# Kernel optimization log

Hardware: AMD Instinct MI355X
Metric: run time of the kernel (lower is better)

The kernel has to match this reference:

```python
import jax, jax.numpy as jnp
import numpy as np
import math

B, N, D, SEQ = 4, 1024, 512, 256
HID, DIST_D, N_NER, N_LAB = 150, 128, 3, 4
SPANS_PER_WORD = 0.5
ASPECT, OPINION = 1, 2
NUM_DIST_EMB = 512


def setup_inputs() -> dict:
    key = jax.random.key(0)
    ks = jax.random.split(key, 9)
    starts = jax.random.randint(ks[0], (B, N), 0, SEQ)
    widths = jax.random.randint(ks[1], (B, N), 0, 8)
    ends = jnp.clip(starts + widths, 0, SEQ - 1)
    spans = jnp.stack([starts, ends], axis=-1).astype(jnp.int32)  # [B,N,2]
    ner_scores = jax.random.normal(ks[2], (B, N, N_NER), jnp.float32)
    span_embeddings = jax.random.normal(ks[3], (B, N, D), jnp.float32)
    span_mask = jnp.ones((B, N), dtype=bool)

    pair_dim = 2 * D + DIST_D

    def xavier(k, shape):
        std = math.sqrt(2.0 / (shape[0] + shape[1]))
        return jax.random.normal(k, shape, jnp.float32) * std

    dist_table = xavier(ks[4], (NUM_DIST_EMB, DIST_D))
    W1 = xavier(ks[5], (pair_dim, HID)); b1 = jnp.zeros((HID,), jnp.float32)
    W2 = xavier(ks[6], (HID, HID));      b2 = jnp.zeros((HID,), jnp.float32)
    Wc = xavier(ks[7], (HID, N_LAB));    bc = jnp.zeros((N_LAB,), jnp.float32)

    return dict(spans=spans, ner_scores=ner_scores, span_embeddings=span_embeddings,
                span_mask=span_mask, seq_length=SEQ, dist_table=dist_table,
                W1=W1, b1=b1, W2=W2, b2=b2, Wc=Wc, bc=bc)


def bucket_values(d, num_identity=4, num_total=10):
    # semi-logscale buckets: [0,1,2,3,4,5-7,8-15,16-31,32-63,64+]
    logspace = jnp.floor(jnp.log2(jnp.maximum(d, 1).astype(jnp.float32))).astype(jnp.int32) + (num_identity - 1)
    return jnp.clip(jnp.where(d <= num_identity, d, logspace), 0, num_total - 1)


def _prune(scores, mask, k):
    masked = jnp.where(mask, scores, jnp.float32(-1e20))
    _, idx = jax.lax.top_k(masked, k)  # [B,k]
    return idx


def reference(spans, ner_scores, span_embeddings, span_mask, seq_length,
              dist_table, W1, b1, W2, b2, Wc, bc):
    bsz, n_spans, d = span_embeddings.shape
    k = min(int(math.ceil(seq_length * SPANS_PER_WORD)), n_spans)

    a_idx = _prune(ner_scores[..., ASPECT], span_mask, k)    # [B,k]
    o_idx = _prune(ner_scores[..., OPINION], span_mask, k)
    a_keep = jnp.ones((bsz, k), dtype=bool)  # uniform seq_length -> all kept
    o_keep = a_keep

    gather = lambda t, i: jnp.take_along_axis(t, i[..., None], axis=1)
    a_emb = gather(span_embeddings, a_idx)   # [B,k,D]
    o_emb = gather(span_embeddings, o_idx)   # [B,k,D]
    spans_a = gather(spans, a_idx)           # [B,k,2]
    spans_o = gather(spans, o_idx)           # [B,k,2]

    # pairwise min span distance -> bucket -> embedding
    dis1 = jnp.abs(spans_a[..., 0][:, :, None] - spans_o[..., 1][:, None, :])
    dis2 = jnp.abs(spans_a[..., 1][:, :, None] - spans_o[..., 0][:, None, :])
    dis = jnp.minimum(dis1, dis2)                      # [B,k,k]
    dist_emb = dist_table[bucket_values(dis)]          # [B,k,k,DIST_D]

    pair = jnp.concatenate([
        jnp.broadcast_to(a_emb[:, :, None, :], (bsz, k, k, d)),
        jnp.broadcast_to(o_emb[:, None, :, :], (bsz, k, k, d)),
        dist_emb,
    ], axis=-1)                                        # [B,k,k,2D+DIST_D]

    # FeedForward (2 layers, ReLU, dropout=identity at eval) + classifier
    h = jax.nn.relu(pair @ W1 + b1)
    h = jax.nn.relu(h @ W2 + b2)
    scores = h @ Wc + bc                               # [B,k,k,n_labels]

    rel_mask = a_keep[:, :, None] & o_keep[:, None, :]
    return (jax.nn.softmax(scores, axis=-1), rel_mask, pair, spans_a, spans_o)
```

## Files before the change

kernel.cpp:

```cpp
#include <hip/hip_runtime.h>
#include <hip/hip_bf16.h>

#define BB 4
#define NN 1024
#define DD 512
#define KK 128
#define HID 150
#define HIDP 160
#define W2TS 176
#define DIST_D 128
#define PAIRD 1152

typedef __attribute__((ext_vector_type(4))) float f32x4;
typedef __attribute__((ext_vector_type(8))) short s16x8;

__device__ __forceinline__ int bucket_of(int dd) {
    return (dd <= 4) ? dd : min(34 - __clz(dd), 9);
}

__global__ __launch_bounds__(256) void k_topk(const int* __restrict__ spans,
                                              const float* __restrict__ ner,
                                              const float* __restrict__ dist_table,
                                              const float* __restrict__ W1,
                                              const float* __restrict__ b1,
                                              const float* __restrict__ W2,
                                              int* ws_aidx, int* ws_oidx,
                                              int* ws_sa, int* ws_so,
                                              float* ws_cd, __hip_bfloat16* ws_w2t,
                                              float* out3, float* out4) {
    int t = threadIdx.x;
    int bx = blockIdx.x;
    if (bx < 32) {
        __shared__ unsigned long long sk[NN];
        int b = bx >> 3;
        int which = (bx >> 2) & 1;
        int chunk = bx & 3;
        int ch = which ? 2 : 1;
#pragma unroll
        for (int k = 0; k < 4; ++k) {
            int d = k * 256 + t;
            float v = ner[(b * NN + d) * 3 + ch];
            unsigned int u = __float_as_uint(v);
            unsigned int s = (u & 0x80000000u) ? ~u : (u ^ 0x80000000u);
            sk[d] = ((unsigned long long)s << 32) | (unsigned int)(NN - 1 - d);
        }
        __syncthreads();
        int idx = chunk * 256 + t;
        unsigned long long mine = sk[idx];
        int cnt = 0;
#pragma unroll 16
        for (int d = 0; d < NN; ++d) cnt += (sk[d] > mine) ? 1 : 0;
        if (cnt < KK) {
            int s0 = spans[(b * NN + idx) * 2];
            int s1 = spans[(b * NN + idx) * 2 + 1];
            int row = b * KK + cnt;
            if (which == 0) {
                ws_aidx[row] = idx;
                ws_sa[row * 2] = s0; ws_sa[row * 2 + 1] = s1;
                out3[row * 2] = (float)s0; out3[row * 2 + 1] = (float)s1;
            } else {
                ws_oidx[row] = idx;
                ws_so[row * 2] = s0; ws_so[row * 2 + 1] = s1;
                out4[row * 2] = (float)s0; out4[row * 2 + 1] = (float)s1;
            }
        }
    } else if (bx < 42) {
        int bk = bx - 32;
        if (t < HIDP) {
            float acc = 0.f;
            if (t < HID) {
                acc = b1[t];
                for (int d = 0; d < DIST_D; ++d)
                    acc = fmaf(dist_table[bk * DIST_D + d], W1[(size_t)(2 * DD + d) * HID + t], acc);
            }
            ws_cd[bk * HIDP + t] = acc;
        }
    } else {
        int e = (bx - 42) * 256 + t;
        if (e < HIDP * W2TS) {
            int n = e / W2TS, d = e - n * W2TS;
            float v = (n < HID && d < HID) ? W2[d * HID + n] : 0.f;
            ws_w2t[e] = __float2bfloat16(v);
        }
    }
}

__global__ __launch_bounds__(256) void k_contrib(const float* __restrict__ emb,
                                                 const float* __restrict__ W1,
                                                 const int* __restrict__ ws_aidx,
                                                 const int* __restrict__ ws_oidx,
                                                 float* ws_ca, float* ws_co) {
    __shared__ __align__(16) float es[4][DD];
    int t = threadIdx.x;
    int bx = blockIdx.x;
    int which = bx >> 7;
    int row0 = (bx & 127) * 4;
    const int* idxsrc = which ? ws_oidx : ws_aidx;
    for (int x = t; x < 512; x += 256) {
        int r = x >> 7, c = x & 127;
        int row = row0 + r;
        int b = row >> 7;
        int idx = idxsrc[row];
        ((float4*)es[r])[c] = ((const float4*)(emb + ((size_t)(b * NN) + idx) * DD))[c];
    }
    __syncthreads();
    if (t < HIDP) {
        float a0 = 0.f, a1 = 0.f, a2 = 0.f, a3 = 0.f;
        if (t < HID) {
            const float* w = W1 + (size_t)(which * DD) * HID + t;
#pragma unroll 4
            for (int d4 = 0; d4 < 128; ++d4) {
                float4 e0 = ((const float4*)es[0])[d4];
                float4 e1 = ((const float4*)es[1])[d4];
                float4 e2 = ((const float4*)es[2])[d4];
                float4 e3 = ((const float4*)es[3])[d4];
                float w0 = w[(size_t)(4 * d4 + 0) * HID];
                float w1v = w[(size_t)(4 * d4 + 1) * HID];
                float w2v = w[(size_t)(4 * d4 + 2) * HID];
                float w3 = w[(size_t)(4 * d4 + 3) * HID];
                a0 = fmaf(e0.x, w0, a0); a0 = fmaf(e0.y, w1v, a0); a0 = fmaf(e0.z, w2v, a0); a0 = fmaf(e0.w, w3, a0);
                a1 = fmaf(e1.x, w0, a1); a1 = fmaf(e1.y, w1v, a1); a1 = fmaf(e1.z, w2v, a1); a1 = fmaf(e1.w, w3, a1);
                a2 = fmaf(e2.x, w0, a2); a2 = fmaf(e2.y, w1v, a2); a2 = fmaf(e2.z, w2v, a2); a2 = fmaf(e2.w, w3, a2);
                a3 = fmaf(e3.x, w0, a3); a3 = fmaf(e3.y, w1v, a3); a3 = fmaf(e3.z, w2v, a3); a3 = fmaf(e3.w, w3, a3);
            }
        }
        float* dstb = which ? ws_co : ws_ca;
        dstb[(row0 + 0) * HIDP + t] = a0;
        dstb[(row0 + 1) * HIDP + t] = a1;
        dstb[(row0 + 2) * HIDP + t] = a2;
        dstb[(row0 + 3) * HIDP + t] = a3;
    }
}

__global__ __launch_bounds__(256, 2) void k_fused(const float* __restrict__ emb,
                                                  const float* __restrict__ dist_table,
                                                  const float* __restrict__ Wc,
                                                  const float* __restrict__ bcp,
                                                  const float* __restrict__ b2p,
                                                  const int* __restrict__ ws_aidx,
                                                  const int* __restrict__ ws_oidx,
                                                  const int* __restrict__ ws_sa,
                                                  const int* __restrict__ ws_so,
                                                  const float* __restrict__ ws_ca,
                                                  const float* __restrict__ ws_co,
                                                  const float* __restrict__ ws_cd,
                                                  const __hip_bfloat16* __restrict__ ws_w2t,
                                                  float* __restrict__ out0,
                                                  float* __restrict__ out1,
                                                  float* __restrict__ out2) {
    int t = threadIdx.x;
    int bx = blockIdx.x;

    if (bx >= 1024) {
        int i = (bx - 1024) * 256 + t;
        ((float4*)out1)[i] = make_float4(1.f, 1.f, 1.f, 1.f);
        return;
    }

    if ((bx & 1) == 0) {
        int bi = bx >> 1;
        int b = bi >> 7;
        int wave = t >> 6, l = t & 63;
        int lc = l & 15, lg = l >> 4;
        int r0 = wave * 32 + lc, r1 = r0 + 16;

        int sa0 = ws_sa[bi * 2], sa1 = ws_sa[bi * 2 + 1];
        int so00 = ws_so[(b * KK + r0) * 2], so01 = ws_so[(b * KK + r0) * 2 + 1];
        int so10 = ws_so[(b * KK + r1) * 2], so11 = ws_so[(b * KK + r1) * 2 + 1];
        int bkt0 = bucket_of(min(abs(sa0 - so01), abs(sa1 - so00)));
        int bkt1 = bucket_of(min(abs(sa0 - so11), abs(sa1 - so10)));

        const f32x4* ca4 = (const f32x4*)(ws_ca + (size_t)bi * HIDP);
        const f32x4* co04 = (const f32x4*)(ws_co + (size_t)(b * KK + r0) * HIDP);
        const f32x4* co14 = (const f32x4*)(ws_co + (size_t)(b * KK + r1) * HIDP);
        const f32x4* cd04 = (const f32x4*)(ws_cd + (size_t)bkt0 * HIDP);
        const f32x4* cd14 = (const f32x4*)(ws_cd + (size_t)bkt1 * HIDP);

        s16x8 af0[5], af1[5];
        union U8 { s16x8 frag; __hip_bfloat16 h[8]; };
#pragma unroll
        for (int kk = 0; kk < 5; ++kk) {
            int o = kk * 8 + lg * 2;
            f32x4 caa = ca4[o], cab = ca4[o + 1];
            f32x4 s0a = caa + co04[o] + cd04[o];
            f32x4 s0b = cab + co04[o + 1] + cd04[o + 1];
            f32x4 s1a = caa + co14[o] + cd14[o];
            f32x4 s1b = cab + co14[o + 1] + cd14[o + 1];
            U8 u0, u1;
#pragma unroll
            for (int e = 0; e < 4; ++e) {
                u0.h[e]     = __float2bfloat16(fmaxf(s0a[e], 0.f));
                u0.h[e + 4] = __float2bfloat16(fmaxf(s0b[e], 0.f));
                u1.h[e]     = __float2bfloat16(fmaxf(s1a[e], 0.f));
                u1.h[e + 4] = __float2bfloat16(fmaxf(s1b[e], 0.f));
            }
            af0[kk] = u0.frag;
            af1[kk] = u1.frag;
        }

        f32x4 acc[2][10];
#pragma unroll
        for (int mi = 0; mi < 2; ++mi)
#pragma unroll
            for (int nt = 0; nt < 10; ++nt)
                acc[mi][nt] = (f32x4){0.f, 0.f, 0.f, 0.f};

#pragma unroll
        for (int kk = 0; kk < 5; ++kk) {
#pragma unroll
            for (int nt = 0; nt < 10; ++nt) {
                s16x8 bf = *(const s16x8*)&ws_w2t[(nt * 16 + lc) * W2TS + kk * 32 + lg * 8];
                acc[0][nt] = __builtin_amdgcn_mfma_f32_16x16x32_bf16(af0[kk], bf, acc[0][nt], 0, 0, 0);
                acc[1][nt] = __builtin_amdgcn_mfma_f32_16x16x32_bf16(af1[kk], bf, acc[1][nt], 0, 0, 0);
            }
        }

        float4 wcv[10];
        float b2v[10];
#pragma unroll
        for (int nt = 0; nt < 10; ++nt) {
            int n = nt * 16 + lc;
            if (n < HID) {
                wcv[nt] = *(const float4*)(Wc + n * 4);
                b2v[nt] = b2p[n];
            } else {
                wcv[nt] = make_float4(0.f, 0.f, 0.f, 0.f);
                b2v[nt] = 0.f;
            }
        }
        float bc0 = bcp[0], bc1 = bcp[1], bc2 = bcp[2], bc3 = bcp[3];

#pragma unroll
        for (int mi = 0; mi < 2; ++mi) {
#pragma unroll
            for (int r = 0; r < 4; ++r) {
                int j = wave * 32 + mi * 16 + lg * 4 + r;
                float p0 = 0.f, p1 = 0.f, p2 = 0.f, p3 = 0.f;
#pragma unroll
                for (int nt = 0; nt < 10; ++nt) {
                    float h2 = fmaxf(acc[mi][nt][r] + b2v[nt], 0.f);
                    p0 = fmaf(h2, wcv[nt].x, p0);
                    p1 = fmaf(h2, wcv[nt].y, p1);
                    p2 = fmaf(h2, wcv[nt].z, p2);
                    p3 = fmaf(h2, wcv[nt].w, p3);
                }
#pragma unroll
                for (int m = 8; m >= 1; m >>= 1) {
                    p0 += __shfl_xor(p0, m, 16);
                    p1 += __shfl_xor(p1, m, 16);
                    p2 += __shfl_xor(p2, m, 16);
                    p3 += __shfl_xor(p3, m, 16);
                }
                p0 += bc0; p1 += bc1; p2 += bc2; p3 += bc3;
                float mx = fmaxf(fmaxf(p0, p1), fmaxf(p2, p3));
                float e0 = expf(p0 - mx), e1 = expf(p1 - mx), e2 = expf(p2 - mx), e3 = expf(p3 - mx);
                float inv = 1.f / (e0 + e1 + e2 + e3);
                if (lc < 4) {
                    float v = (lc == 0) ? e0 : (lc == 1) ? e1 : (lc == 2) ? e2 : e3;
                    out0[((size_t)bi * KK + j) * 4 + lc] = v * inv;
                }
            }
        }
    } else {
        int pid = bx >> 1;
        int b = pid >> 7;
        int ig = (pid >> 2) & 31;
        int jc = pid & 3;
        int i0 = ig << 2;
        int j0 = jc << 5;
        int c = t & 127;
        int half = t >> 7;

        const f32x4* ebase = (const f32x4*)(emb + (size_t)b * NN * DD);

        f32x4 areg[4];
#pragma unroll
        for (int ii = 0; ii < 4; ++ii) {
            int aidx = ws_aidx[b * KK + i0 + ii];
            areg[ii] = ebase[(size_t)aidx * 128 + c];
        }

        f32x4 oreg[16];
#pragma unroll
        for (int it = 0; it < 16; ++it) {
            int j = it * 2 + half;
            int oidx = ws_oidx[b * KK + j0 + j];
            oreg[it] = ebase[(size_t)oidx * 128 + c];
        }

        int dj[4], dc[4], so0v[4], so1v[4];
#pragma unroll
        for (int it = 0; it < 4; ++it) {
            int x = it * 256 + t;
            dj[it] = x >> 5; dc[it] = x & 31;
            so0v[it] = ws_so[(b * KK + j0 + dj[it]) * 2];
            so1v[it] = ws_so[(b * KK + j0 + dj[it]) * 2 + 1];
        }
        f32x4 dreg[4][4];
#pragma unroll
        for (int ii = 0; ii < 4; ++ii) {
            int sa0 = ws_sa[(b * KK + i0 + ii) * 2];
            int sa1 = ws_sa[(b * KK + i0 + ii) * 2 + 1];
#pragma unroll
            for (int it = 0; it < 4; ++it) {
                int bkt = bucket_of(min(abs(sa0 - so1v[it]), abs(sa1 - so0v[it])));
                dreg[ii][it] = ((const f32x4*)dist_table)[bkt * 32 + dc[it]];
            }
        }

#pragma unroll
        for (int ii = 0; ii < 4; ++ii) {
            f32x4* dst = (f32x4*)(out2 + (size_t)(b * KK + i0 + ii) * (KK * PAIRD))
                         + (size_t)j0 * 288;
#pragma unroll
            for (int it = 0; it < 16; ++it) {
                int j = it * 2 + half;
                dst[j * 288 + c] = areg[ii];
                dst[j * 288 + 128 + c] = oreg[it];
            }
#pragma unroll
            for (int it = 0; it < 4; ++it)
                dst[dj[it] * 288 + 256 + dc[it]] = dreg[ii][it];
        }
    }
}

extern "C" void kernel_launch(void* const* d_in, const int* in_sizes, int n_in,
                              void* d_out, int out_size, void* d_ws, size_t ws_size,
                              hipStream_t stream) {
    const int*   spans = (const int*)d_in[0];
    const float* ner   = (const float*)d_in[1];
    const float* emb   = (const float*)d_in[2];
    const float* dist_table = (const float*)d_in[5];
    const float* W1 = (const float*)d_in[6];
    const float* b1 = (const float*)d_in[7];
    const float* W2 = (const float*)d_in[8];
    const float* b2 = (const float*)d_in[9];
    const float* Wc = (const float*)d_in[10];
    const float* bc = (const float*)d_in[11];

    float* out0 = (float*)d_out;
    float* out1 = out0 + (size_t)BB * KK * KK * 4;
    float* out2 = out1 + (size_t)BB * KK * KK;
    float* out3 = out2 + (size_t)BB * KK * KK * PAIRD;
    float* out4 = out3 + (size_t)BB * KK * 2;

    int* ws_aidx = (int*)d_ws;
    int* ws_oidx = ws_aidx + BB * KK;
    int* ws_sa   = ws_oidx + BB * KK;
    int* ws_so   = ws_sa + BB * KK * 2;
    float* ws_ca = (float*)(ws_so + BB * KK * 2);
    float* ws_co = ws_ca + BB * KK * HIDP;
    float* ws_cd = ws_co + BB * KK * HIDP;
    __hip_bfloat16* ws_w2t = (__hip_bfloat16*)(ws_cd + 16 * HIDP);

    k_topk<<<152, 256, 0, stream>>>(spans, ner, dist_table, W1, b1, W2,
                                    ws_aidx, ws_oidx, ws_sa, ws_so,
                                    ws_cd, ws_w2t, out3, out4);
    k_contrib<<<256, 256, 0, stream>>>(emb, W1, ws_aidx, ws_oidx, ws_ca, ws_co);
    k_fused<<<1088, 256, 0, stream>>>(emb, dist_table, Wc, bc, b2,
                                      ws_aidx, ws_oidx, ws_sa, ws_so,
                                      ws_ca, ws_co, ws_cd, ws_w2t,
                                      out0, out1, out2);
}
```

Baseline: 97.95 us.

## Rebalance pair-tensor writes across middle and main kernels to overlap with contrib

The pair-tensor materialisation is moved into a shared device function. A quarter of its blocks (128), plus the ones-mask fill, now run in the middle kernel alongside the W1 contribution GEMV, which by itself only used 256 blocks. The remaining 384 pair blocks run first in the main kernel, ahead of the MFMA classifier blocks, which are no longer interleaved with them. The aim is to fill idle CUs during the small contrib kernel and shorten the main kernel, at the cost of a heavier middle kernel whose pair blocks use more registers (launch_bounds 256,2).

```diff
diff --git a/kernel.cpp b/kernel.cpp
--- a/kernel.cpp
+++ b/kernel.cpp
@@ -16,6 +16,75 @@
 
 __device__ __forceinline__ int bucket_of(int dd) {
     return (dd <= 4) ? dd : min(34 - __clz(dd), 9);
+}
+
+__device__ __forceinline__ void pair_body(int pid, int t,
+                                          const float* __restrict__ emb,
+                                          const float* __restrict__ dist_table,
+                                          const int* __restrict__ ws_aidx,
+                                          const int* __restrict__ ws_oidx,
+                                          const int* __restrict__ ws_sa,
+                                          const int* __restrict__ ws_so,
+                                          float* __restrict__ out2) {
+    int b = pid >> 7;
+    int ig = (pid >> 2) & 31;
+    int jc = pid & 3;
+    int i0 = ig << 2;
+    int j0 = jc << 5;
+    int c = t & 127;
+    int half = t >> 7;
+
+    const f32x4* ebase = (const f32x4*)(emb + (size_t)b * NN * DD);
+
+    f32x4 areg[4];
+#pragma unroll
+    for (int ii = 0; ii < 4; ++ii) {
+        int aidx = ws_aidx[b * KK + i0 + ii];
+        areg[ii] = ebase[(size_t)aidx * 128 + c];
+    }
+
+    f32x4 oreg[16];
+#pragma unroll
+    for (int it = 0; it < 16; ++it) {
+        int j = it * 2 + half;
+        int oidx = ws_oidx[b * KK + j0 + j];
+        oreg[it] = ebase[(size_t)oidx * 128 + c];
+    }
+
+    int dj[4], dc[4], so0v[4], so1v[4];
+#pragma unroll
+    for (int it = 0; it < 4; ++it) {
+        int x = it * 256 + t;
+        dj[it] = x >> 5; dc[it] = x & 31;
+        so0v[it] = ws_so[(b * KK + j0 + dj[it]) * 2];
+        so1v[it] = ws_so[(b * KK + j0 + dj[it]) * 2 + 1];
+    }
+    f32x4 dreg[4][4];
+#pragma unroll
+    for (int ii = 0; ii < 4; ++ii) {
+        int sa0 = ws_sa[(b * KK + i0 + ii) * 2];
+        int sa1 = ws_sa[(b * KK + i0 + ii) * 2 + 1];
+#pragma unroll
+        for (int it = 0; it < 4; ++it) {
+            int bkt = bucket_of(min(abs(sa0 - so1v[it]), abs(sa1 - so0v[it])));
+            dreg[ii][it] = ((const f32x4*)dist_table)[bkt * 32 + dc[it]];
+        }
+    }
+
+#pragma unroll
+    for (int ii = 0; ii < 4; ++ii) {
+        f32x4* dst = (f32x4*)(out2 + (size_t)(b * KK + i0 + ii) * (KK * PAIRD))
+                     + (size_t)j0 * 288;
+#pragma unroll
+        for (int it = 0; it < 16; ++it) {
+            int j = it * 2 + half;
+            dst[j * 288 + c] = areg[ii];
+            dst[j * 288 + 128 + c] = oreg[it];
+        }
+#pragma unroll
+        for (int it = 0; it < 4; ++it)
+            dst[dj[it] * 288 + 256 + dc[it]] = dreg[ii][it];
+    }
 }
 
 __global__ __launch_bounds__(256) void k_topk(const int* __restrict__ spans,
@@ -85,16 +154,33 @@
     }
 }
 
-__global__ __launch_bounds__(256) void k_contrib(const float* __restrict__ emb,
-                                                 const float* __restrict__ W1,
-                                                 const int* __restrict__ ws_aidx,
-                                                 const int* __restrict__ ws_oidx,
-                                                 float* ws_ca, float* ws_co) {
+__global__ __launch_bounds__(256, 2) void k_mid(const float* __restrict__ emb,
+                                                const float* __restrict__ dist_table,
+                                                const float* __restrict__ W1,
+                                                const int* __restrict__ ws_aidx,
+                                                const int* __restrict__ ws_oidx,
+                                                const int* __restrict__ ws_sa,
+                                                const int* __restrict__ ws_so,
+                                                float* ws_ca, float* ws_co,
+                                                float* __restrict__ out1,
+                                                float* __restrict__ out2) {
     __shared__ __align__(16) float es[4][DD];
     int t = threadIdx.x;
     int bx = blockIdx.x;
-    int which = bx >> 7;
-    int row0 = (bx & 127) * 4;
+
+    if (bx < 128) {
+        pair_body(bx, t, emb, dist_table, ws_aidx, ws_oidx, ws_sa, ws_so, out2);
+        return;
+    }
+    if (bx >= 384) {
+        int i = (bx - 384) * 256 + t;
+        ((float4*)out1)[i] = make_float4(1.f, 1.f, 1.f, 1.f);
+        return;
+    }
+
+    int cbx = bx - 128;
+    int which = cbx >> 7;
+    int row0 = (cbx & 127) * 4;
     const int* idxsrc = which ? ws_oidx : ws_aidx;
     for (int x = t; x < 512; x += 256) {
         int r = x >> 7, c = x & 127;
@@ -132,195 +218,130 @@
     }
 }
 
-__global__ __launch_bounds__(256, 2) void k_fused(const float* __restrict__ emb,
-                                                  const float* __restrict__ dist_table,
-                                                  const float* __restrict__ Wc,
-                                                  const float* __restrict__ bcp,
-                                                  const float* __restrict__ b2p,
-                                                  const int* __restrict__ ws_aidx,
-                                                  const int* __restrict__ ws_oidx,
-                                                  const int* __restrict__ ws_sa,
-                                                  const int* __restrict__ ws_so,
-                                                  const float* __restrict__ ws_ca,
-                                                  const float* __restrict__ ws_co,
-                                                  const float* __restrict__ ws_cd,
-                                                  const __hip_bfloat16* __restrict__ ws_w2t,
-                                                  float* __restrict__ out0,
-                                                  float* __restrict__ out1,
-                                                  float* __restrict__ out2) {
+__global__ __launch_bounds__(256, 2) void k_main(const float* __restrict__ emb,
+                                                 const float* __restrict__ dist_table,
+                                                 const float* __restrict__ Wc,
+                                                 const float* __restrict__ bcp,
+                                                 const float* __restrict__ b2p,
+                                                 const int* __restrict__ ws_aidx,
+                                                 const int* __restrict__ ws_oidx,
+                                                 const int* __restrict__ ws_sa,
+                                                 const int* __restrict__ ws_so,
+                                                 const float* __restrict__ ws_ca,
+                                                 const float* __restrict__ ws_co,
+                                                 const float* __restrict__ ws_cd,
+                                                 const __hip_bfloat16* __restrict__ ws_w2t,
+                                                 float* __restrict__ out0,
+                                                 float* __restrict__ out2) {
     int t = threadIdx.x;
     int bx = blockIdx.x;
 
-    if (bx >= 1024) {
-        int i = (bx - 1024) * 256 + t;
-        ((float4*)out1)[i] = make_float4(1.f, 1.f, 1.f, 1.f);
+    if (bx < 384) {
+        pair_body(128 + bx, t, emb, dist_table, ws_aidx, ws_oidx, ws_sa, ws_so, out2);
         return;
     }
 
-    if ((bx & 1) == 0) {
-        int bi = bx >> 1;
-        int b = bi >> 7;
-        int wave = t >> 6, l = t & 63;
-        int lc = l & 15, lg = l >> 4;
-        int r0 = wave * 32 + lc, r1 = r0 + 16;
-
-        int sa0 = ws_sa[bi * 2], sa1 = ws_sa[bi * 2 + 1];
-        int so00 = ws_so[(b * KK + r0) * 2], so01 = ws_so[(b * KK + r0) * 2 + 1];
-        int so10 = ws_so[(b * KK + r1) * 2], so11 = ws_so[(b * KK + r1) * 2 + 1];
-        int bkt0 = bucket_of(min(abs(sa0 - so01), abs(sa1 - so00)));
-        int bkt1 = bucket_of(min(abs(sa0 - so11), abs(sa1 - so10)));
-
-        const f32x4* ca4 = (const f32x4*)(ws_ca + (size_t)bi * HIDP);
-        const f32x4* co04 = (const f32x4*)(ws_co + (size_t)(b * KK + r0) * HIDP);
-        const f32x4* co14 = (const f32x4*)(ws_co + (size_t)(b * KK + r1) * HIDP);
-        const f32x4* cd04 = (const f32x4*)(ws_cd + (size_t)bkt0 * HIDP);
-        const f32x4* cd14 = (const f32x4*)(ws_cd + (size_t)bkt1 * HIDP);
-
-        s16x8 af0[5], af1[5];
-        union U8 { s16x8 frag; __hip_bfloat16 h[8]; };
-#pragma unroll
-        for (int kk = 0; kk < 5; ++kk) {
-            int o = kk * 8 + lg * 2;
-            f32x4 caa = ca4[o], cab = ca4[o + 1];
-            f32x4 s0a = caa + co04[o] + cd04[o];
-            f32x4 s0b = cab + co04[o + 1] + cd04[o + 1];
-            f32x4 s1a = caa + co14[o] + cd14[o];
-            f32x4 s1b = cab + co14[o + 1] + cd14[o + 1];
-            U8 u0, u1;
-#pragma unroll
-            for (int e = 0; e < 4; ++e) {
-                u0.h[e]     = __float2bfloat16(fmaxf(s0a[e], 0.f));
-                u0.h[e + 4] = __float2bfloat16(fmaxf(s0b[e], 0.f));
-                u1.h[e]     = __float2bfloat16(fmaxf(s1a[e], 0.f));
-                u1.h[e + 4] = __float2bfloat16(fmaxf(s1b[e], 0.f));
-            }
-            af0[kk] = u0.frag;
-            af1[kk] = u1.frag;
-        }
-
-        f32x4 acc[2][10];
-#pragma unroll
-        for (int mi = 0; mi < 2; ++mi)
-#pragma unroll
-            for (int nt = 0; nt < 10; ++nt)
-                acc[mi][nt] = (f32x4){0.f, 0.f, 0.f, 0.f};
-
-#pragma unroll
-        for (int kk = 0; kk < 5; ++kk) {
+    int bi = bx - 384;
+    int b = bi >> 7;
+    int wave = t >> 6, l = t & 63;
+    int lc = l & 15, lg = l >> 4;
+    int r0 = wave * 32 + lc, r1 = r0 + 16;
+
+    int sa0 = ws_sa[bi * 2], sa1 = ws_sa[bi * 2 + 1];
+    int so00 = ws_so[(b * KK + r0) * 2], so01 = ws_so[(b * KK + r0) * 2 + 1];
+    int so10 = ws_so[(b * KK + r1) * 2], so11 = ws_so[(b * KK + r1) * 2 + 1];
+    int bkt0 = bucket_of(min(abs(sa0 - so01), abs(sa1 - so00)));
+    int bkt1 = bucket_of(min(abs(sa0 - so11), abs(sa1 - so10)));
+
+    const f32x4* ca4 = (const f32x4*)(ws_ca + (size_t)bi * HIDP);
+    const f32x4* co04 = (const f32x4*)(ws_co + (size_t)(b * KK + r0) * HIDP);
+    const f32x4* co14 = (const f32x4*)(ws_co + (size_t)(b * KK + r1) * HIDP);
+    const f32x4* cd04 = (const f32x4*)(ws_cd + (size_t)bkt0 * HIDP);
+    const f32x4* cd14 = (const f32x4*)(ws_cd + (size_t)bkt1 * HIDP);
+
+    s16x8 af0[5], af1[5];
+    union U8 { s16x8 frag; __hip_bfloat16 h[8]; };
+#pragma unroll
+    for (int kk = 0; kk < 5; ++kk) {
+        int o = kk * 8 + lg * 2;
+        f32x4 caa = ca4[o], cab = ca4[o + 1];
+        f32x4 s0a = caa + co04[o] + cd04[o];
+        f32x4 s0b = cab + co04[o + 1] + cd04[o + 1];
+        f32x4 s1a = caa + co14[o] + cd14[o];
+        f32x4 s1b = cab + co14[o + 1] + cd14[o + 1];
+        U8 u0, u1;
+#pragma unroll
+        for (int e = 0; e < 4; ++e) {
+            u0.h[e]     = __float2bfloat16(fmaxf(s0a[e], 0.f));
+            u0.h[e + 4] = __float2bfloat16(fmaxf(s0b[e], 0.f));
+            u1.h[e]     = __float2bfloat16(fmaxf(s1a[e], 0.f));
+            u1.h[e + 4] = __float2bfloat16(fmaxf(s1b[e], 0.f));
+        }
+        af0[kk] = u0.frag;
+        af1[kk] = u1.frag;
+    }
+
+    f32x4 acc[2][10];
+#pragma unroll
+    for (int mi = 0; mi < 2; ++mi)
+#pragma unroll
+        for (int nt = 0; nt < 10; ++nt)
+            acc[mi][nt] = (f32x4){0.f, 0.f, 0.f, 0.f};
+
+#pragma unroll
+    for (int kk = 0; kk < 5; ++kk) {
+#pragma unroll
+        for (int nt = 0; nt < 10; ++nt) {
+            s16x8 bf = *(const s16x8*)&ws_w2t[(nt * 16 + lc) * W2TS + kk * 32 + lg * 8];
+            acc[0][nt] = __builtin_amdgcn_mfma_f32_16x16x32_bf16(af0[kk], bf, acc[0][nt], 0, 0, 0);
+            acc[1][nt] = __builtin_amdgcn_mfma_f32_16x16x32_bf16(af1[kk], bf, acc[1][nt], 0, 0, 0);
+        }
+    }
+
+    float4 wcv[10];
+    float b2v[10];
+#pragma unroll
+    for (int nt = 0; nt < 10; ++nt) {
+        int n = nt * 16 + lc;
+        if (n < HID) {
+            wcv[nt] = *(const float4*)(Wc + n * 4);
+            b2v[nt] = b2p[n];
+        } else {
+            wcv[nt] = make_float4(0.f, 0.f, 0.f, 0.f);
+            b2v[nt] = 0.f;
+        }
+    }
+    float bc0 = bcp[0], bc1 = bcp[1], bc2 = bcp[2], bc3 = bcp[3];
+
+#pragma unroll
+    for (int mi = 0; mi < 2; ++mi) {
+#pragma unroll
+        for (int r = 0; r < 4; ++r) {
+            int j = wave * 32 + mi * 16 + lg * 4 + r;
+            float p0 = 0.f, p1 = 0.f, p2 = 0.f, p3 = 0.f;
 #pragma unroll
             for (int nt = 0; nt < 10; ++nt) {
-                s16x8 bf = *(const s16x8*)&ws_w2t[(nt * 16 + lc) * W2TS + kk * 32 + lg * 8];
-                acc[0][nt] = __builtin_amdgcn_mfma_f32_16x16x32_bf16(af0[kk], bf, acc[0][nt], 0, 0, 0);
-                acc[1][nt] = __builtin_amdgcn_mfma_f32_16x16x32_bf16(af1[kk], bf, acc[1][nt], 0, 0, 0);
-            }
-        }
-
-        float4 wcv[10];
-        float b2v[10];
-#pragma unroll
-        for (int nt = 0; nt < 10; ++nt) {
-            int n = nt * 16 + lc;
-            if (n < HID) {
-                wcv[nt] = *(const float4*)(Wc + n * 4);
-                b2v[nt] = b2p[n];
-            } else {
-                wcv[nt] = make_float4(0.f, 0.f, 0.f, 0.f);
-                b2v[nt] = 0.f;
-            }
-        }
-        float bc0 = bcp[0], bc1 = bcp[1], bc2 = bcp[2], bc3 = bcp[3];
-
-#pragma unroll
-        for (int mi = 0; mi < 2; ++mi) {
-#pragma unroll
-            for (int r = 0; r < 4; ++r) {
-                int j = wave * 32 + mi * 16 + lg * 4 + r;
-                float p0 = 0.f, p1 = 0.f, p2 = 0.f, p3 = 0.f;
-#pragma unroll
-                for (int nt = 0; nt < 10; ++nt) {
-                    float h2 = fmaxf(acc[mi][nt][r] + b2v[nt], 0.f);
-                    p0 = fmaf(h2, wcv[nt].x, p0);
-                    p1 = fmaf(h2, wcv[nt].y, p1);
-                    p2 = fmaf(h2, wcv[nt].z, p2);
-                    p3 = fmaf(h2, wcv[nt].w, p3);
-                }
-#pragma unroll
-                for (int m = 8; m >= 1; m >>= 1) {
-                    p0 += __shfl_xor(p0, m, 16);
-                    p1 += __shfl_xor(p1, m, 16);
-                    p2 += __shfl_xor(p2, m, 16);
-                    p3 += __shfl_xor(p3, m, 16);
-                }
-                p0 += bc0; p1 += bc1; p2 += bc2; p3 += bc3;
-                float mx = fmaxf(fmaxf(p0, p1), fmaxf(p2, p3));
-                float e0 = expf(p0 - mx), e1 = expf(p1 - mx), e2 = expf(p2 - mx), e3 = expf(p3 - mx);
-                float inv = 1.f / (e0 + e1 + e2 + e3);
-                if (lc < 4) {
-                    float v = (lc == 0) ? e0 : (lc == 1) ? e1 : (lc == 2) ? e2 : e3;
-                    out0[((size_t)bi * KK + j) * 4 + lc] = v * inv;
-                }
-            }
-        }
-    } else {
-        int pid = bx >> 1;
-        int b = pid >> 7;
-        int ig = (pid >> 2) & 31;
-        int jc = pid & 3;
-        int i0 = ig << 2;
-        int j0 = jc << 5;
-        int c = t & 127;
-        int half = t >> 7;
-
-        const f32x4* ebase = (const f32x4*)(emb + (size_t)b * NN * DD);
-
-        f32x4 areg[4];
-#pragma unroll
-        for (int ii = 0; ii < 4; ++ii) {
-            int aidx = ws_aidx[b * KK + i0 + ii];
-            areg[ii] = ebase[(size_t)aidx * 128 + c];
-        }
-
-        f32x4 oreg[16];
-#pragma unroll
-        for (int it = 0; it < 16; ++it) {
-            int j = it * 2 + half;
-            int oidx = ws_oidx[b * KK + j0 + j];
-            oreg[it] = ebase[(size_t)oidx * 128 + c];
-        }
-
-        int dj[4], dc[4], so0v[4], so1v[4];
-#pragma unroll
-        for (int it = 0; it < 4; ++it) {
-            int x = it * 256 + t;
-            dj[it] = x >> 5; dc[it] = x & 31;
-            so0v[it] = ws_so[(b * KK + j0 + dj[it]) * 2];
-            so1v[it] = ws_so[(b * KK + j0 + dj[it]) * 2 + 1];
-        }
-        f32x4 dreg[4][4];
-#pragma unroll
-        for (int ii = 0; ii < 4; ++ii) {
-            int sa0 = ws_sa[(b * KK + i0 + ii) * 2];
-            int sa1 = ws_sa[(b * KK + i0 + ii) * 2 + 1];
-#pragma unroll
-            for (int it = 0; it < 4; ++it) {
-                int bkt = bucket_of(min(abs(sa0 - so1v[it]), abs(sa1 - so0v[it])));
-                dreg[ii][it] = ((const f32x4*)dist_table)[bkt * 32 + dc[it]];
-            }
-        }
-
-#pragma unroll
-        for (int ii = 0; ii < 4; ++ii) {
-            f32x4* dst = (f32x4*)(out2 + (size_t)(b * KK + i0 + ii) * (KK * PAIRD))
-                         + (size_t)j0 * 288;
-#pragma unroll
-            for (int it = 0; it < 16; ++it) {
-                int j = it * 2 + half;
-                dst[j * 288 + c] = areg[ii];
-                dst[j * 288 + 128 + c] = oreg[it];
-            }
-#pragma unroll
-            for (int it = 0; it < 4; ++it)
-                dst[dj[it] * 288 + 256 + dc[it]] = dreg[ii][it];
+                float h2 = fmaxf(acc[mi][nt][r] + b2v[nt], 0.f);
+                p0 = fmaf(h2, wcv[nt].x, p0);
+                p1 = fmaf(h2, wcv[nt].y, p1);
+                p2 = fmaf(h2, wcv[nt].z, p2);
+                p3 = fmaf(h2, wcv[nt].w, p3);
+            }
+#pragma unroll
+            for (int m = 8; m >= 1; m >>= 1) {
+                p0 += __shfl_xor(p0, m, 16);
+                p1 += __shfl_xor(p1, m, 16);
+                p2 += __shfl_xor(p2, m, 16);
+                p3 += __shfl_xor(p3, m, 16);
+            }
+            p0 += bc0; p1 += bc1; p2 += bc2; p3 += bc3;
+            float mx = fmaxf(fmaxf(p0, p1), fmaxf(p2, p3));
+            float e0 = expf(p0 - mx), e1 = expf(p1 - mx), e2 = expf(p2 - mx), e3 = expf(p3 - mx);
+            float inv = 1.f / (e0 + e1 + e2 + e3);
+            if (lc < 4) {
+                float v = (lc == 0) ? e0 : (lc == 1) ? e1 : (lc == 2) ? e2 : e3;
+                out0[((size_t)bi * KK + j) * 4 + lc] = v * inv;
+            }
         }
     }
 }
@@ -357,9 +378,11 @@
     k_topk<<<152, 256, 0, stream>>>(spans, ner, dist_table, W1, b1, W2,
                                     ws_aidx, ws_oidx, ws_sa, ws_so,
                                     ws_cd, ws_w2t, out3, out4);
-    k_contrib<<<256, 256, 0, stream>>>(emb, W1, ws_aidx, ws_oidx, ws_ca, ws_co);
-    k_fused<<<1088, 256, 0, stream>>>(emb, dist_table, Wc, bc, b2,
-                                      ws_aidx, ws_oidx, ws_sa, ws_so,
-                                      ws_ca, ws_co, ws_cd, ws_w2t,
-                                      out0, out1, out2);
-}
+    k_mid<<<448, 256, 0, stream>>>(emb, dist_table, W1,
+                                   ws_aidx, ws_oidx, ws_sa, ws_so,
+                                   ws_ca, ws_co, out1, out2);
+    k_main<<<896, 256, 0, stream>>>(emb, dist_table, Wc, bc, b2,
+                                    ws_aidx, ws_oidx, ws_sa, ws_so,
+                                    ws_ca, ws_co, ws_cd, ws_w2t,
+                                    out0, out2);
+}
```

After: 97.30 us. Within noise of the previous version (-0.7%).
